# Kernel tuning notes

Measured on AMD Instinct MI355X. Metric: run time of the kernel, lower is better.

The kernel has to match this reference:

```python
import jax, jax.numpy as jnp
import numpy as np

DIM = 512
NUM_HEADS = 8
HEAD_DIM = DIM // NUM_HEADS
KERNEL = (3, 5, 5)  # (kd, kh, kw), must be odd and <= spatial dims
B, D, H, W = 1, 6, 48, 96


def setup_inputs() -> dict:
    key = jax.random.key(0)
    ks = jax.random.split(key, 5)
    x = jax.random.normal(ks[0], (B, D, H, W, DIM), jnp.float32)
    w_qkv = jax.random.normal(ks[1], (DIM, 3 * DIM), jnp.float32) * 0.02
    b_qkv = jax.random.normal(ks[2], (3 * DIM,), jnp.float32) * 0.02
    w_proj = jax.random.normal(ks[3], (DIM, DIM), jnp.float32) * 0.02
    b_proj = jax.random.normal(ks[4], (DIM,), jnp.float32) * 0.02
    return {"x": x, "w_qkv": w_qkv, "b_qkv": b_qkv, "w_proj": w_proj, "b_proj": b_proj}


def _nbhd_idx(L, k):
    # NATTEN neighborhood: window of exactly k keys, centered, shifted inward at edges.
    p = jnp.arange(L)
    start = jnp.clip(p - k // 2, 0, L - k)
    return start[:, None] + jnp.arange(k)[None, :]  # [L, k]


def _na3d(q, k, v, kernel):
    # q, k, v: [B, D, H, W, heads, hd]; q pre-scaled.
    kd, kh, kw = kernel
    _, Dd, Hh, Ww, _, _ = q.shape
    idx_d = _nbhd_idx(Dd, kd)
    idx_h = _nbhd_idx(Hh, kh)
    idx_w = _nbhd_idx(Ww, kw)
    offs = jnp.stack(
        jnp.meshgrid(jnp.arange(kd), jnp.arange(kh), jnp.arange(kw), indexing="ij"),
        axis=-1,
    ).reshape(-1, 3)  # [K3, 3]

    def shift(t, o):
        # gather the o-th neighbor of every query position along each spatial axis
        t = jnp.take(t, jnp.take(idx_d, o[0], axis=1), axis=1)
        t = jnp.take(t, jnp.take(idx_h, o[1], axis=1), axis=2)
        t = jnp.take(t, jnp.take(idx_w, o[2], axis=1), axis=3)
        return t

    def score_step(_, o):
        k_s = shift(k, o)
        s = jnp.einsum("bdhwnc,bdhwnc->bdhwn", q, k_s)
        return None, s

    _, scores = jax.lax.scan(score_step, None, offs)  # [K3, B, D, H, W, heads]
    attn = jax.nn.softmax(scores, axis=0)

    def out_step(acc, xs):
        o, a = xs
        v_s = shift(v, o)
        return acc + a[..., None] * v_s, None

    out, _ = jax.lax.scan(out_step, jnp.zeros_like(q), (offs, attn))
    return out


def reference(x, w_qkv, b_qkv, w_proj, b_proj):
    Bb, Dd, Hh, Ww, C = x.shape
    qkv = (x @ w_qkv + b_qkv).reshape(Bb, Dd, Hh, Ww, 3, NUM_HEADS, HEAD_DIM)
    q = qkv[..., 0, :, :]
    k = qkv[..., 1, :, :]
    v = qkv[..., 2, :, :]
    scale = HEAD_DIM ** (-0.5)
    # Faithful to source: module scales q by self.scale, then tuned_na3d applies
    # head_dim**-0.5 again inside the fused kernel -> net q * head_dim**-1.
    q = q * (scale * scale)
    out = _na3d(q, k, v, KERNEL).reshape(Bb, Dd, Hh, Ww, C)
    return out @ w_proj + b_proj
```

## Files before the change

### kernel.cpp

```cpp
#include <hip/hip_runtime.h>

#define DIMC   512
#define NHEADS 8
#define HDIM   64
#define DD     6
#define HHH    48
#define WWW    96
#define NPOS   (DD * HHH * WWW)

typedef unsigned short u16;
typedef __attribute__((ext_vector_type(8))) short bf16x8;
typedef __attribute__((ext_vector_type(4))) float f32x4;

static __device__ __forceinline__ float b2f(u16 u) {
    return __builtin_bit_cast(float, (unsigned)u << 16);
}
static __device__ __forceinline__ u16 f2b(float f) {
    unsigned x = __builtin_bit_cast(unsigned, f);
    return (u16)((x + 0x7fffu + ((x >> 16) & 1u)) >> 16);
}

static __device__ __forceinline__ void gload_lds16(const void* g, void* l) {
    __builtin_amdgcn_global_load_lds((const __attribute__((address_space(1))) void*)g,
                                     (__attribute__((address_space(3))) void*)l, 16, 0, 0);
}

__global__ __launch_bounds__(256) void cvt_x_bf16(const float* __restrict__ in,
                                                  u16* __restrict__ out, int n4) {
    const int i = blockIdx.x * 256 + threadIdx.x;
    float4 v = reinterpret_cast<const float4*>(in)[i];
    ushort4 o = { f2b(v.x), f2b(v.y), f2b(v.z), f2b(v.w) };
    reinterpret_cast<ushort4*>(out)[i] = o;
}

__global__ __launch_bounds__(256) void cvt_wqkvT(const float* __restrict__ w,
                                                 u16* __restrict__ o) {
    const int id = blockIdx.x * 256 + threadIdx.x;
    const int nn = id >> 9, kk = id & 511;
    o[id] = f2b(w[(size_t)kk * 1536 + nn]);
}

__global__ __launch_bounds__(256) void cvt_wprojT(const float* __restrict__ w,
                                                  u16* __restrict__ o) {
    const int id = blockIdx.x * 256 + threadIdx.x;
    const int nn = id >> 9, kk = id & 511;
    o[id] = f2b(w[(size_t)kk * 512 + nn]);
}

__global__ __launch_bounds__(256) void gemm_bf16_mfma(
    const u16* __restrict__ A, int lda,
    const u16* __restrict__ B, int ldb,
    const float* __restrict__ bias, int Kp,
    void* __restrict__ Cout, int ldc, int cmode, int nx)
{
    __shared__ u16 As[128 * 64];
    __shared__ u16 Bs[128 * 64];

    const int tid = threadIdx.x;
    const int l   = tid & 63;
    const int w   = tid >> 6;
    const int wr  = w >> 1, wc = w & 1;

    const int cpx = gridDim.x >> 3;
    const int idp = (blockIdx.x & 7) * cpx + (blockIdx.x >> 3);
    const int by  = idp / nx;
    const int bx  = idp - by * nx;
    const int m0  = by * 128;
    const int n0  = bx * 128;

    const int srow = tid >> 3;
    const int schk = ((tid & 7) ^ (srow & 7)) * 8;

    const u16* ga = A + (size_t)(m0 + srow) * lda + schk;
    const u16* gb = B + (size_t)(n0 + srow) * ldb + schk;
    const size_t a32 = (size_t)32 * lda;
    const size_t b32 = (size_t)32 * ldb;
    u16* const la0 = As + (w * 8) * 64;
    u16* const lb0 = Bs + (w * 8) * 64;

    f32x4 acc[4][4];
#pragma unroll
    for (int i = 0; i < 4; i++)
#pragma unroll
        for (int j = 0; j < 4; j++) acc[i][j] = (f32x4)0.0f;

    const int c   = l & 15;
    const int g   = l >> 4;
    const int lk0 = (((0 * 4 + g) ^ (c & 7))) * 8;
    const int lk1 = (((1 * 4 + g) ^ (c & 7))) * 8;

#pragma unroll 1
    for (int k0 = 0; k0 < Kp; k0 += 64) {
#pragma unroll
        for (int q = 0; q < 4; ++q) {
            gload_lds16(ga + q * a32, la0 + q * 32 * 64);
            gload_lds16(gb + q * b32, lb0 + q * 32 * 64);
        }
        ga += 64; gb += 64;
        __syncthreads();

        {
            bf16x8 af[4], bfr[4];
#pragma unroll
            for (int f = 0; f < 4; f++) {
                af[f]  = *reinterpret_cast<const bf16x8*>(&As[(wr * 64 + f * 16 + c) * 64 + lk0]);
                bfr[f] = *reinterpret_cast<const bf16x8*>(&Bs[(wc * 64 + f * 16 + c) * 64 + lk0]);
            }
#pragma unroll
            for (int i = 0; i < 4; i++)
#pragma unroll
                for (int j = 0; j < 4; j++)
                    acc[i][j] = __builtin_amdgcn_mfma_f32_16x16x32_bf16(af[i], bfr[j], acc[i][j], 0, 0, 0);
        }
        {
            bf16x8 af[4], bfr[4];
#pragma unroll
            for (int f = 0; f < 4; f++) {
                af[f]  = *reinterpret_cast<const bf16x8*>(&As[(wr * 64 + f * 16 + c) * 64 + lk1]);
                bfr[f] = *reinterpret_cast<const bf16x8*>(&Bs[(wc * 64 + f * 16 + c) * 64 + lk1]);
            }
#pragma unroll
            for (int i = 0; i < 4; i++)
#pragma unroll
                for (int j = 0; j < 4; j++)
                    acc[i][j] = __builtin_amdgcn_mfma_f32_16x16x32_bf16(af[i], bfr[j], acc[i][j], 0, 0, 0);
        }
        __syncthreads();
    }

#pragma unroll
    for (int i = 0; i < 4; i++) {
        const int mb = m0 + wr * 64 + i * 16 + g * 4;
#pragma unroll
        for (int j = 0; j < 4; j++) {
            const int n = n0 + wc * 64 + j * 16 + c;
            const float bv = bias[n];
#pragma unroll
            for (int r = 0; r < 4; r++) {
                const float v = acc[i][j][r] + bv;
                if (cmode) reinterpret_cast<u16*>(Cout)[(size_t)(mb + r) * ldc + n] = f2b(v);
                else       reinterpret_cast<float*>(Cout)[(size_t)(mb + r) * ldc + n] = v;
            }
        }
    }
}

__global__ __launch_bounds__(512, 4) void na3d_mfma(
    const u16* __restrict__ qkv, u16* __restrict__ attnc)
{
    __shared__ int   rowoff[192];
    __shared__ int   dlt[16];
    __shared__ u16   Pbuf[NHEADS][16][36];
    __shared__ u16   Vt[NHEADS][64][36];
    __shared__ float ssum_lds[NHEADS][16];

    const int bid  = blockIdx.x;
    const int tile = (bid & 7) * 216 + (bid >> 3);
    const int pd  = tile / 288;
    const int rem = tile - pd * 288;
    const int h0  = (rem / 24) * 4;
    const int w0  = (rem % 24) * 4;
    const int sd  = min(max(pd - 1, 0), DD - 3);
    const int shb = min(max(h0 - 2, 0), HHH - 5);
    const int swb = min(max(w0 - 2, 0), WWW - 5);

    const int tid = threadIdx.x;
    if (tid < 192) {
        const int dd = tid >> 6, hh = (tid >> 3) & 7, wu = tid & 7;
        const int row = (sd + dd) * (HHH * WWW)
                      + min(shb + hh, HHH - 1) * WWW + min(swb + wu, WWW - 1);
        rowoff[tid] = row * 1536;
    }
    if (tid < 16) {
        const int ph = h0 + (tid >> 2), pw = w0 + (tid & 3);
        const int dh = min(max(ph - 2, 0), HHH - 5) - shb;
        const int dw = min(max(pw - 2, 0), WWW - 5) - swb;
        dlt[tid] = (dh << 4) | dw;
    }
    __syncthreads();

    const int head = tid >> 6;
    const int l    = tid & 63;
    const int g    = l >> 4;
    const int c    = l & 15;

    const int qrowi = pd * (HHH * WWW) + (h0 + (c >> 2)) * WWW + (w0 + (c & 3));
    const u16* qrow = qkv + (size_t)qrowi * 1536 + head * HDIM;
    const bf16x8 qlo = *reinterpret_cast<const bf16x8*>(qrow + 8 * g);
    const bf16x8 qhi = *reinterpret_cast<const bf16x8*>(qrow + 32 + 8 * g);
    const int dparts = dlt[c];
    const int dh = dparts >> 4, dw = dparts & 15;

    f32x4 oacc[4];
#pragma unroll
    for (int j = 0; j < 4; j++) oacc[j] = (f32x4)0.0f;
    float ssum = 0.0f;

    const float SC = 0.022542110f;

#pragma unroll 1
    for (int s = 0; s < 6; ++s) {
        {
            const int npair = l >> 2;
            const int chq   = l & 3;
#pragma unroll
            for (int rr = 0; rr < 2; ++rr) {
                const int ch8 = 8 * chq + 32 * rr;
                const int2 rp = *reinterpret_cast<const int2*>(&rowoff[s * 32 + 2 * npair]);
                const ushort4* pa = reinterpret_cast<const ushort4*>(qkv + rp.x + 1024 + head * HDIM + ch8);
                const ushort4* pb = reinterpret_cast<const ushort4*>(qkv + rp.y + 1024 + head * HDIM + ch8);
                ushort4 va0 = pa[0], va1 = pa[1];
                ushort4 vb0 = pb[0], vb1 = pb[1];
                const u16* va = reinterpret_cast<const u16*>(&va0);
                const u16* vb = reinterpret_cast<const u16*>(&vb0);
#pragma unroll
                for (int e = 0; e < 4; ++e) {
                    unsigned dwo = (unsigned)va[e] | ((unsigned)vb[e] << 16);
                    *reinterpret_cast<unsigned*>(&Vt[head][ch8 + e][2 * npair]) = dwo;
                }
                const u16* va2 = reinterpret_cast<const u16*>(&va1);
                const u16* vb2 = reinterpret_cast<const u16*>(&vb1);
#pragma unroll
                for (int e = 0; e < 4; ++e) {
                    unsigned dwo = (unsigned)va2[e] | ((unsigned)vb2[e] << 16);
                    *reinterpret_cast<unsigned*>(&Vt[head][ch8 + 4 + e][2 * npair]) = dwo;
                }
            }
        }

#pragma unroll
        for (int t = 0; t < 2; ++t) {
            const int sb0 = s * 32 + t * 16;
            const int ro  = rowoff[sb0 + c];
            const u16* kr = qkv + ro + 512 + head * HDIM;
            const bf16x8 klo = *reinterpret_cast<const bf16x8*>(kr + 8 * g);
            const bf16x8 khi = *reinterpret_cast<const bf16x8*>(kr + 32 + 8 * g);
            f32x4 sf = (f32x4)0.0f;
            sf = __builtin_amdgcn_mfma_f32_16x16x32_bf16(klo, qlo, sf, 0, 0, 0);
            sf = __builtin_amdgcn_mfma_f32_16x16x32_bf16(khi, qhi, sf, 0, 0, 0);
            const int sb  = sb0 + 4 * g;
            const int wu0 = sb & 7;
            const int hh_ = (sb >> 3) & 7;
            const bool hv = ((unsigned)(hh_ - dh) < 5u);
            float e0, e1, e2, e3;
            e0 = (hv && (unsigned)(wu0 + 0 - dw) < 5u) ? exp2f(sf[0] * SC) : 0.0f;
            e1 = (hv && (unsigned)(wu0 + 1 - dw) < 5u) ? exp2f(sf[1] * SC) : 0.0f;
            e2 = (hv && (unsigned)(wu0 + 2 - dw) < 5u) ? exp2f(sf[2] * SC) : 0.0f;
            e3 = (hv && (unsigned)(wu0 + 3 - dw) < 5u) ? exp2f(sf[3] * SC) : 0.0f;
            ssum += e0 + e1 + e2 + e3;
            const unsigned p01 = (unsigned)f2b(e0) | ((unsigned)f2b(e1) << 16);
            const unsigned p23 = (unsigned)f2b(e2) | ((unsigned)f2b(e3) << 16);
            *reinterpret_cast<unsigned*>(&Pbuf[head][c][t * 16 + 4 * g])     = p01;
            *reinterpret_cast<unsigned*>(&Pbuf[head][c][t * 16 + 4 * g + 2]) = p23;
        }

        {
            const uint2 p01 = *reinterpret_cast<const uint2*>(&Pbuf[head][c][8 * g]);
            const uint2 p23 = *reinterpret_cast<const uint2*>(&Pbuf[head][c][8 * g + 4]);
            const int4 pv = make_int4((int)p01.x, (int)p01.y, (int)p23.x, (int)p23.y);
            const bf16x8 pfrag = __builtin_bit_cast(bf16x8, pv);
#pragma unroll
            for (int j = 0; j < 4; ++j) {
                const uint2 v01 = *reinterpret_cast<const uint2*>(&Vt[head][16 * j + c][8 * g]);
                const uint2 v23 = *reinterpret_cast<const uint2*>(&Vt[head][16 * j + c][8 * g + 4]);
                const int4 vv = make_int4((int)v01.x, (int)v01.y, (int)v23.x, (int)v23.y);
                const bf16x8 vfrag = __builtin_bit_cast(bf16x8, vv);
                oacc[j] = __builtin_amdgcn_mfma_f32_16x16x32_bf16(pfrag, vfrag, oacc[j], 0, 0, 0);
            }
        }
    }

    ssum += __shfl_xor(ssum, 16);
    ssum += __shfl_xor(ssum, 32);
    if (l < 16) ssum_lds[head][c] = ssum;
    const f32x4 sums4 = *reinterpret_cast<const f32x4*>(&ssum_lds[head][4 * g]);

    const int orow = pd * (HHH * WWW) + (h0 + g) * WWW + w0;
#pragma unroll
    for (int r = 0; r < 4; ++r) {
        const float inv = 1.0f / sums4[r];
        u16* base = attnc + (size_t)(orow + r) * 512 + head * HDIM;
#pragma unroll
        for (int j = 0; j < 4; ++j)
            base[16 * j + c] = f2b(oacc[j][r] * inv);
    }
}

extern "C" void kernel_launch(void* const* d_in, const int* in_sizes, int n_in,
                              void* d_out, int out_size, void* d_ws, size_t ws_size,
                              hipStream_t stream)
{
    const float* x      = (const float*)d_in[0];
    const float* w_qkv  = (const float*)d_in[1];
    const float* b_qkv  = (const float*)d_in[2];
    const float* w_proj = (const float*)d_in[3];
    const float* b_proj = (const float*)d_in[4];
    float* out = (float*)d_out;

    u16* qkvb   = (u16*)d_ws;
    u16* attnc  = qkvb  + (size_t)NPOS * 1536;
    u16* xb     = attnc + (size_t)NPOS * 512;
    u16* wqkvT  = xb    + (size_t)NPOS * 512;
    u16* wprojT = wqkvT + (size_t)1536 * 512;

    cvt_x_bf16<<<(NPOS * 512 / 4) / 256, 256, 0, stream>>>(x, xb, NPOS * 512 / 4);
    cvt_wqkvT<<<(1536 * 512) / 256, 256, 0, stream>>>(w_qkv, wqkvT);
    cvt_wprojT<<<(512 * 512) / 256, 256, 0, stream>>>(w_proj, wprojT);

    gemm_bf16_mfma<<<(1536 / 128) * (NPOS / 128), 256, 0, stream>>>(
        xb, 512, wqkvT, 512, b_qkv, 512, qkvb, 1536, 1, 1536 / 128);

    na3d_mfma<<<NPOS / 16, 512, 0, stream>>>(qkvb, attnc);

    gemm_bf16_mfma<<<(512 / 128) * (NPOS / 128), 256, 0, stream>>>(
        attnc, 512, wprojT, 512, b_proj, 512, out, 512, 0, 512 / 128);
}
```

Before: 186.7 us.

## Software-pipeline K/V global loads one stage ahead in neighborhood attention loop

The attention main loop now uses two register sets and prefetches the K and V rows for the next stage while the current stage's QK^T, softmax and PV MFMAs run. The loop is unrolled by two stages. The aim is to hide global-memory latency behind compute. In exchange it raises register pressure, which could lower occupancy, and issues one redundant prefetch of the last stage.

Result: no change. 187.4 us (+0.4%).

```diff
diff --git a/kernel.cpp b/kernel.cpp
--- a/kernel.cpp
+++ b/kernel.cpp
@@ -179,10 +179,12 @@
     }
     __syncthreads();
 
-    const int head = tid >> 6;
-    const int l    = tid & 63;
-    const int g    = l >> 4;
-    const int c    = l & 15;
+    const int head  = tid >> 6;
+    const int l     = tid & 63;
+    const int g     = l >> 4;
+    const int c     = l & 15;
+    const int npair = l >> 2;
+    const int chq   = l & 3;
 
     const int qrowi = pd * (HHH * WWW) + (h0 + (c >> 2)) * WWW + (w0 + (c & 3));
     const u16* qrow = qkv + (size_t)qrowi * 1536 + head * HDIM;
@@ -191,6 +193,8 @@
     const int dparts = dlt[c];
     const int dh = dparts >> 4, dw = dparts & 15;
 
+    const u16* const vbase = qkv + 1024 + head * HDIM + 8 * chq;
+
     f32x4 oacc[4];
 #pragma unroll
     for (int j = 0; j < 4; j++) oacc[j] = (f32x4)0.0f;
@@ -198,77 +202,112 @@
 
     const float SC = 0.022542110f;
 
+#define LOADK_(sn, KL0, KH0, KL1, KH1) do {                                    \
+    const int roA = rowoff[(sn) * 32 + c];                                     \
+    const int roB = rowoff[(sn) * 32 + 16 + c];                                \
+    const u16* krA = qkv + roA + 512 + head * HDIM;                            \
+    const u16* krB = qkv + roB + 512 + head * HDIM;                            \
+    KL0 = *reinterpret_cast<const bf16x8*>(krA + 8 * g);                       \
+    KH0 = *reinterpret_cast<const bf16x8*>(krA + 32 + 8 * g);                  \
+    KL1 = *reinterpret_cast<const bf16x8*>(krB + 8 * g);                       \
+    KH1 = *reinterpret_cast<const bf16x8*>(krB + 32 + 8 * g);                  \
+} while (0)
+
+#define LOADV_(sn, V0, V1, V2, V3, V4, V5, V6, V7) do {                        \
+    const int2 rp = *reinterpret_cast<const int2*>(&rowoff[(sn) * 32 + 2 * npair]); \
+    const ushort4* pa = reinterpret_cast<const ushort4*>(vbase + rp.x);        \
+    const ushort4* pb = reinterpret_cast<const ushort4*>(vbase + rp.y);        \
+    V0 = pa[0]; V1 = pa[1]; V2 = pb[0]; V3 = pb[1];                            \
+    V4 = pa[8]; V5 = pa[9]; V6 = pb[8]; V7 = pb[9];                            \
+} while (0)
+
+#define PACK4_(rowbase, VA, VB) do {                                           \
+    const u16* _a = reinterpret_cast<const u16*>(&(VA));                       \
+    const u16* _b = reinterpret_cast<const u16*>(&(VB));                       \
+    *reinterpret_cast<unsigned*>(&Vt[head][(rowbase) + 0][2 * npair]) = (unsigned)_a[0] | ((unsigned)_b[0] << 16); \
+    *reinterpret_cast<unsigned*>(&Vt[head][(rowbase) + 1][2 * npair]) = (unsigned)_a[1] | ((unsigned)_b[1] << 16); \
+    *reinterpret_cast<unsigned*>(&Vt[head][(rowbase) + 2][2 * npair]) = (unsigned)_a[2] | ((unsigned)_b[2] << 16); \
+    *reinterpret_cast<unsigned*>(&Vt[head][(rowbase) + 3][2 * npair]) = (unsigned)_a[3] | ((unsigned)_b[3] << 16); \
+} while (0)
+
+#define WRITEV_(V0, V1, V2, V3, V4, V5, V6, V7) do {                           \
+    PACK4_(8 * chq,      V0, V2);                                              \
+    PACK4_(8 * chq + 4,  V1, V3);                                              \
+    PACK4_(8 * chq + 32, V4, V6);                                              \
+    PACK4_(8 * chq + 36, V5, V7);                                              \
+} while (0)
+
+#define QKT_(s, t, KLO, KHI) do {                                              \
+    f32x4 sf = (f32x4)0.0f;                                                    \
+    sf = __builtin_amdgcn_mfma_f32_16x16x32_bf16(KLO, qlo, sf, 0, 0, 0);       \
+    sf = __builtin_amdgcn_mfma_f32_16x16x32_bf16(KHI, qhi, sf, 0, 0, 0);       \
+    const int sb  = (s) * 32 + (t) * 16 + 4 * g;                               \
+    const int wu0 = sb & 7;                                                    \
+    const int hh_ = (sb >> 3) & 7;                                             \
+    const bool hv = ((unsigned)(hh_ - dh) < 5u);                               \
+    const float e0 = (hv && (unsigned)(wu0 + 0 - dw) < 5u) ? exp2f(sf[0] * SC) : 0.0f; \
+    const float e1 = (hv && (unsigned)(wu0 + 1 - dw) < 5u) ? exp2f(sf[1] * SC) : 0.0f; \
+    const float e2 = (hv && (unsigned)(wu0 + 2 - dw) < 5u) ? exp2f(sf[2] * SC) : 0.0f; \
+    const float e3 = (hv && (unsigned)(wu0 + 3 - dw) < 5u) ? exp2f(sf[3] * SC) : 0.0f; \
+    ssum += e0 + e1 + e2 + e3;                                                 \
+    const unsigned p01 = (unsigned)f2b(e0) | ((unsigned)f2b(e1) << 16);        \
+    const unsigned p23 = (unsigned)f2b(e2) | ((unsigned)f2b(e3) << 16);        \
+    *reinterpret_cast<unsigned*>(&Pbuf[head][c][(t) * 16 + 4 * g])     = p01;  \
+    *reinterpret_cast<unsigned*>(&Pbuf[head][c][(t) * 16 + 4 * g + 2]) = p23;  \
+} while (0)
+
+#define PV_() do {                                                             \
+    const uint2 p01 = *reinterpret_cast<const uint2*>(&Pbuf[head][c][8 * g]);  \
+    const uint2 p23 = *reinterpret_cast<const uint2*>(&Pbuf[head][c][8 * g + 4]); \
+    const int4 pv = make_int4((int)p01.x, (int)p01.y, (int)p23.x, (int)p23.y); \
+    const bf16x8 pfrag = __builtin_bit_cast(bf16x8, pv);                       \
+    const uint2 v01a = *reinterpret_cast<const uint2*>(&Vt[head][c][8 * g]);   \
+    const uint2 v23a = *reinterpret_cast<const uint2*>(&Vt[head][c][8 * g + 4]); \
+    oacc[0] = __builtin_amdgcn_mfma_f32_16x16x32_bf16(pfrag, __builtin_bit_cast(bf16x8, make_int4((int)v01a.x, (int)v01a.y, (int)v23a.x, (int)v23a.y)), oacc[0], 0, 0, 0); \
+    const uint2 v01b = *reinterpret_cast<const uint2*>(&Vt[head][16 + c][8 * g]); \
+    const uint2 v23b = *reinterpret_cast<const uint2*>(&Vt[head][16 + c][8 * g + 4]); \
+    oacc[1] = __builtin_amdgcn_mfma_f32_16x16x32_bf16(pfrag, __builtin_bit_cast(bf16x8, make_int4((int)v01b.x, (int)v01b.y, (int)v23b.x, (int)v23b.y)), oacc[1], 0, 0, 0); \
+    const uint2 v01c = *reinterpret_cast<const uint2*>(&Vt[head][32 + c][8 * g]); \
+    const uint2 v23c = *reinterpret_cast<const uint2*>(&Vt[head][32 + c][8 * g + 4]); \
+    oacc[2] = __builtin_amdgcn_mfma_f32_16x16x32_bf16(pfrag, __builtin_bit_cast(bf16x8, make_int4((int)v01c.x, (int)v01c.y, (int)v23c.x, (int)v23c.y)), oacc[2], 0, 0, 0); \
+    const uint2 v01d = *reinterpret_cast<const uint2*>(&Vt[head][48 + c][8 * g]); \
+    const uint2 v23d = *reinterpret_cast<const uint2*>(&Vt[head][48 + c][8 * g + 4]); \
+    oacc[3] = __builtin_amdgcn_mfma_f32_16x16x32_bf16(pfrag, __builtin_bit_cast(bf16x8, make_int4((int)v01d.x, (int)v01d.y, (int)v23d.x, (int)v23d.y)), oacc[3], 0, 0, 0); \
+} while (0)
+
+    bf16x8 xk0, xk1, xk2, xk3, yk0, yk1, yk2, yk3;
+    ushort4 xv0, xv1, xv2, xv3, xv4, xv5, xv6, xv7;
+    ushort4 yv0, yv1, yv2, yv3, yv4, yv5, yv6, yv7;
+
+    LOADK_(0, xk0, xk1, xk2, xk3);
+    LOADV_(0, xv0, xv1, xv2, xv3, xv4, xv5, xv6, xv7);
+
 #pragma unroll 1
-    for (int s = 0; s < 6; ++s) {
-        {
-            const int npair = l >> 2;
-            const int chq   = l & 3;
-#pragma unroll
-            for (int rr = 0; rr < 2; ++rr) {
-                const int ch8 = 8 * chq + 32 * rr;
-                const int2 rp = *reinterpret_cast<const int2*>(&rowoff[s * 32 + 2 * npair]);
-                const ushort4* pa = reinterpret_cast<const ushort4*>(qkv + rp.x + 1024 + head * HDIM + ch8);
-                const ushort4* pb = reinterpret_cast<const ushort4*>(qkv + rp.y + 1024 + head * HDIM + ch8);
-                ushort4 va0 = pa[0], va1 = pa[1];
-                ushort4 vb0 = pb[0], vb1 = pb[1];
-                const u16* va = reinterpret_cast<const u16*>(&va0);
-                const u16* vb = reinterpret_cast<const u16*>(&vb0);
-#pragma unroll
-                for (int e = 0; e < 4; ++e) {
-                    unsigned dwo = (unsigned)va[e] | ((unsigned)vb[e] << 16);
-                    *reinterpret_cast<unsigned*>(&Vt[head][ch8 + e][2 * npair]) = dwo;
-                }
-                const u16* va2 = reinterpret_cast<const u16*>(&va1);
-                const u16* vb2 = reinterpret_cast<const u16*>(&vb1);
-#pragma unroll
-                for (int e = 0; e < 4; ++e) {
-                    unsigned dwo = (unsigned)va2[e] | ((unsigned)vb2[e] << 16);
-                    *reinterpret_cast<unsigned*>(&Vt[head][ch8 + 4 + e][2 * npair]) = dwo;
-                }
-            }
-        }
-
-#pragma unroll
-        for (int t = 0; t < 2; ++t) {
-            const int sb0 = s * 32 + t * 16;
-            const int ro  = rowoff[sb0 + c];
-            const u16* kr = qkv + ro + 512 + head * HDIM;
-            const bf16x8 klo = *reinterpret_cast<const bf16x8*>(kr + 8 * g);
-            const bf16x8 khi = *reinterpret_cast<const bf16x8*>(kr + 32 + 8 * g);
-            f32x4 sf = (f32x4)0.0f;
-            sf = __builtin_amdgcn_mfma_f32_16x16x32_bf16(klo, qlo, sf, 0, 0, 0);
-            sf = __builtin_amdgcn_mfma_f32_16x16x32_bf16(khi, qhi, sf, 0, 0, 0);
-            const int sb  = sb0 + 4 * g;
-            const int wu0 = sb & 7;
-            const int hh_ = (sb >> 3) & 7;
-            const bool hv = ((unsigned)(hh_ - dh) < 5u);
-            float e0, e1, e2, e3;
-            e0 = (hv && (unsigned)(wu0 + 0 - dw) < 5u) ? exp2f(sf[0] * SC) : 0.0f;
-            e1 = (hv && (unsigned)(wu0 + 1 - dw) < 5u) ? exp2f(sf[1] * SC) : 0.0f;
-            e2 = (hv && (unsigned)(wu0 + 2 - dw) < 5u) ? exp2f(sf[2] * SC) : 0.0f;
-            e3 = (hv && (unsigned)(wu0 + 3 - dw) < 5u) ? exp2f(sf[3] * SC) : 0.0f;
-            ssum += e0 + e1 + e2 + e3;
-            const unsigned p01 = (unsigned)f2b(e0) | ((unsigned)f2b(e1) << 16);
-            const unsigned p23 = (unsigned)f2b(e2) | ((unsigned)f2b(e3) << 16);
-            *reinterpret_cast<unsigned*>(&Pbuf[head][c][t * 16 + 4 * g])     = p01;
-            *reinterpret_cast<unsigned*>(&Pbuf[head][c][t * 16 + 4 * g + 2]) = p23;
-        }
-
-        {
-            const uint2 p01 = *reinterpret_cast<const uint2*>(&Pbuf[head][c][8 * g]);
-            const uint2 p23 = *reinterpret_cast<const uint2*>(&Pbuf[head][c][8 * g + 4]);
-            const int4 pv = make_int4((int)p01.x, (int)p01.y, (int)p23.x, (int)p23.y);
-            const bf16x8 pfrag = __builtin_bit_cast(bf16x8, pv);
-#pragma unroll
-            for (int j = 0; j < 4; ++j) {
-                const uint2 v01 = *reinterpret_cast<const uint2*>(&Vt[head][16 * j + c][8 * g]);
-                const uint2 v23 = *reinterpret_cast<const uint2*>(&Vt[head][16 * j + c][8 * g + 4]);
-                const int4 vv = make_int4((int)v01.x, (int)v01.y, (int)v23.x, (int)v23.y);
-                const bf16x8 vfrag = __builtin_bit_cast(bf16x8, vv);
-                oacc[j] = __builtin_amdgcn_mfma_f32_16x16x32_bf16(pfrag, vfrag, oacc[j], 0, 0, 0);
-            }
-        }
-    }
+    for (int i = 0; i < 3; ++i) {
+        const int s0 = 2 * i, s1 = 2 * i + 1;
+        const int s2 = (s1 < 5) ? s1 + 1 : 5;
+
+        WRITEV_(xv0, xv1, xv2, xv3, xv4, xv5, xv6, xv7);
+        LOADV_(s1, yv0, yv1, yv2, yv3, yv4, yv5, yv6, yv7);
+        LOADK_(s1, yk0, yk1, yk2, yk3);
+        QKT_(s0, 0, xk0, xk1);
+        QKT_(s0, 1, xk2, xk3);
+        PV_();
+
+        WRITEV_(yv0, yv1, yv2, yv3, yv4, yv5, yv6, yv7);
+        LOADV_(s2, xv0, xv1, xv2, xv3, xv4, xv5, xv6, xv7);
+        LOADK_(s2, xk0, xk1, xk2, xk3);
+        QKT_(s1, 0, yk0, yk1);
+        QKT_(s1, 1, yk2, yk3);
+        PV_();
+    }
+
+#undef LOADK_
+#undef LOADV_
+#undef PACK4_
+#undef WRITEV_
+#undef QKT_
+#undef PV_
 
     ssum += __shfl_xor(ssum, 16);
     ssum += __shfl_xor(ssum, 32);
```
